# Kernel optimization log

Hardware: AMD Instinct MI355X
Metric: run time of the kernel (lower is better)

## Reference

```python
import jax, jax.numpy as jnp
import numpy as np

B, T, E, H = 4, 8192, 1024, 16
D = E // H
SCALE = 1.0 / np.sqrt(D).astype(np.float32)
EPS_FM = 1e-6
EPS_Z = 1e-8


def setup_inputs() -> dict:
    key = jax.random.key(0)
    ks = jax.random.split(key, 11)
    s = 1.0 / np.sqrt(E).astype(np.float32)  # small init so feature map stays sane
    return {
        'query': jax.random.normal(ks[0], (B, T, E), jnp.float32),
        'key': jax.random.normal(ks[1], (B, T, E), jnp.float32),
        'value': jax.random.normal(ks[2], (B, T, E), jnp.float32),
        'Wq': jax.random.normal(ks[3], (E, E), jnp.float32) * s,
        'bq': jax.random.normal(ks[4], (E,), jnp.float32) * 0.01,
        'Wk': jax.random.normal(ks[5], (E, E), jnp.float32) * s,
        'bk': jax.random.normal(ks[6], (E,), jnp.float32) * 0.01,
        'Wv': jax.random.normal(ks[7], (E, E), jnp.float32) * s,
        'bv': jax.random.normal(ks[8], (E,), jnp.float32) * 0.01,
        'Wo': jax.random.normal(ks[9], (E, E), jnp.float32) * s,
        'bo': jax.random.normal(ks[10], (E,), jnp.float32) * 0.01,
    }


def _heads(x):
    # (B, T, E) -> (B, H, T, D)
    b, t, _ = x.shape
    return x.reshape(b, t, H, D).transpose(0, 2, 1, 3)


def _feature_map(x):
    return jax.nn.relu(x) + EPS_FM


def reference(query, key, value, Wq, bq, Wk, bk, Wv, bv, Wo, bo):
    b, tq, _ = query.shape
    Q = _feature_map(_heads(query @ Wq.T + bq) * SCALE)  # (B,H,Tq,D)
    K = _feature_map(_heads(key @ Wk.T + bk) * SCALE)    # (B,H,Tk,D)
    V = _heads(value @ Wv.T + bv)                         # (B,H,Tk,D)
    KV = jnp.einsum('bhnd,bhne->bhde', K, V)              # (B,H,D,D)
    K_sum = K.sum(axis=2)                                 # (B,H,D)
    Z = jnp.einsum('bhnd,bhd->bhn', Q, K_sum) + EPS_Z     # (B,H,Tq)
    out = jnp.einsum('bhnd,bhde->bhne', Q, KV) / Z[..., None]
    out = out.transpose(0, 2, 1, 3).reshape(b, tq, E)
    return out @ Wo.T + bo
```

## Files before the change

### kernel.cpp

```cpp
#include <hip/hip_runtime.h>
#include <hip/hip_bf16.h>


#define SCALE_ 0.125f
#define EPS_FM_ 1e-6f
#define EPS_Z_ 1e-8f

typedef __bf16 bf16;
typedef __attribute__((ext_vector_type(4))) __bf16 bf16x4;
typedef __attribute__((ext_vector_type(8))) __bf16 bf16x8;
typedef __attribute__((ext_vector_type(8))) unsigned short u16x8;
typedef __attribute__((ext_vector_type(4))) float f32x4;

__device__ __forceinline__ void gl_lds16(const void* g, void* l) {
  __builtin_amdgcn_global_load_lds(
      (const __attribute__((address_space(1))) void*)g,
      (__attribute__((address_space(3))) void*)l, 16, 0, 0);
}

#define SBAR()                                  \
  do {                                          \
    __builtin_amdgcn_sched_barrier(0);          \
    asm volatile("s_barrier" ::: "memory");     \
    __builtin_amdgcn_sched_barrier(0);          \
  } while (0)

__global__ __launch_bounds__(256) void cast_weights(
    const float* __restrict__ Wq, const float* __restrict__ Wk,
    const float* __restrict__ Wv, const float* __restrict__ Wo,
    bf16* __restrict__ out) {
  int which = blockIdx.y;
  int j = (blockIdx.x * 256 + threadIdx.x) * 4;
  const float* s = (which == 0) ? Wq : (which == 1) ? Wk : (which == 2) ? Wv : Wo;
  float4 v = *(const float4*)(s + j);
  bf16x4 p = {(bf16)v.x, (bf16)v.y, (bf16)v.z, (bf16)v.w};
  *(bf16x4*)(out + (size_t)which * (1u << 20) + j) = p;
}

template <int MODE>
__global__ __launch_bounds__(512, 2) void gemm8p(
    const bf16* __restrict__ Ab, const float* __restrict__ Aq,
    const float* __restrict__ Ak, const float* __restrict__ Av,
    const bf16* __restrict__ Wb, const float* __restrict__ b0,
    const float* __restrict__ b1, const float* __restrict__ b2,
    bf16* __restrict__ Pb, float* __restrict__ Pf) {
  __shared__ __align__(16) char lds[65536];
  const int tid = threadIdx.x;
  const int bid = blockIdx.x;
  const int wg = (bid & 7) * (gridDim.x >> 3) + (bid >> 3);
  const int mt = wg >> 2;
  int seg = 0, om = 2;
  if constexpr (MODE == 0) {
    seg = mt >> 7;
    om = (seg < 2) ? 0 : 1;
  }
  const int m0 = (MODE == 0 ? (mt & 127) : mt) * 256;
  const int n0 = (wg & 3) * 256;
  const int wave = tid >> 6, lane = tid & 63;
  const int wm = wave >> 2, wn = wave & 3;
  const int l16 = lane & 15, kg = lane >> 4;
  const int e = l16 & 7;
  const int sw0 = (kg ^ e) << 4;
  const int sw1 = ((4 | kg) ^ e) << 4;

  const int tr = tid >> 3;
  const int cslot = (tid & 7) ^ (tr & 7);
  const bf16* pA = nullptr;
  const float* pAf = nullptr;
  if constexpr (MODE == 1)
    pA = Ab + (size_t)(m0 + tr) * 1024 + cslot * 8;
  else {
    const float* Af = (seg == 0) ? Aq : (seg == 1) ? Ak : Av;
    pAf = Af + (size_t)(m0 + tr) * 1024 + cslot * 8;
  }
  const bf16* W = (MODE == 0) ? Wb + ((size_t)seg << 20) : Wb;
  const float* bias = (MODE == 0) ? ((seg == 0) ? b0 : (seg == 1) ? b1 : b2) : b0;
  const bf16* pB = W + (size_t)(n0 + ((tr >> 5) << 6) + (tr & 31)) * 1024 + cslot * 8;
  char* sA = lds;
  char* sB = lds + 32768;

  auto stgA = [&](int h, int kt) {
    const bf16* g = pA + h * 65536 + kt * 64;
    char* d = sA + h * 16384 + tid * 16;
    gl_lds16(g, d);
    gl_lds16(g + 131072, d + 8192);
  };
  auto stgB = [&](int h, int kt) {
    const bf16* g = pB + h * 32768 + kt * 64;
    char* d = sB + h * 16384 + tid * 16;
    gl_lds16(g, d);
    gl_lds16(g + 131072, d + 8192);
  };
  auto ldgA = [&](int h, int kt, f32x4* r) {
    const float* g = pAf + h * 65536 + kt * 64;
    r[0] = *(const f32x4*)g;
    r[1] = *(const f32x4*)(g + 4);
    r[2] = *(const f32x4*)(g + 131072);
    r[3] = *(const f32x4*)(g + 131072 + 4);
  };
  auto wrA = [&](int h, const f32x4* r) {
    bf16x8 p0 = {(bf16)r[0][0], (bf16)r[0][1], (bf16)r[0][2], (bf16)r[0][3],
                 (bf16)r[1][0], (bf16)r[1][1], (bf16)r[1][2], (bf16)r[1][3]};
    bf16x8 p1 = {(bf16)r[2][0], (bf16)r[2][1], (bf16)r[2][2], (bf16)r[2][3],
                 (bf16)r[3][0], (bf16)r[3][1], (bf16)r[3][2], (bf16)r[3][3]};
    char* d = sA + h * 16384 + tid * 16;
    *(bf16x8*)d = p0;
    *(bf16x8*)(d + 8192) = p1;
  };

  const int aBase = wm * 8192 + l16 * 128;
  const int bBase = wn * 4096 + l16 * 128;
  auto ldA = [&](int h, int fmi, int kk) {
    return *(const bf16x8*)(sA + h * 16384 + aBase + fmi * 2048 +
                            (kk ? sw1 : sw0));
  };
  auto ldB = [&](int h, int fnj, int kk) {
    return *(const bf16x8*)(sB + h * 16384 + bBase + fnj * 2048 +
                            (kk ? sw1 : sw0));
  };

  f32x4 acc[8][4] = {};
  bf16x8 rA[4][2], rB01[2][2], rB23[2][2];
  f32x4 ga[4], gb[4];
  const int NT = 16;

  if constexpr (MODE == 1) {
    stgA(0, 0); stgB(0, 0); stgB(1, 0); stgA(1, 0);
    asm volatile("s_waitcnt vmcnt(2)" ::: "memory");
  } else {
    ldgA(0, 0, ga); ldgA(1, 0, gb);
    stgB(0, 0); stgB(1, 0);
    asm volatile("s_waitcnt vmcnt(12)" ::: "memory");
    wrA(0, ga);
    asm volatile("s_waitcnt vmcnt(4)" ::: "memory");
    wrA(1, gb);
    ldgA(0, 1, ga); ldgA(1, 1, gb);
    asm volatile("s_waitcnt vmcnt(16)" ::: "memory");
    asm volatile("s_waitcnt lgkmcnt(0)" ::: "memory");
  }
  SBAR();

#pragma unroll 2
  for (int t = 0; t < NT; ++t) {
#pragma unroll
    for (int fmi = 0; fmi < 4; ++fmi) {
      rA[fmi][0] = ldA(0, fmi, 0);
      rA[fmi][1] = ldA(0, fmi, 1);
    }
#pragma unroll
    for (int fnj = 0; fnj < 2; ++fnj) {
      rB01[fnj][0] = ldB(0, fnj, 0);
      rB01[fnj][1] = ldB(0, fnj, 1);
    }
    SBAR();
    __builtin_amdgcn_s_setprio(1);
#pragma unroll
    for (int fmi = 0; fmi < 4; ++fmi)
#pragma unroll
      for (int fnj = 0; fnj < 2; ++fnj)
#pragma unroll
        for (int kk = 0; kk < 2; ++kk)
          acc[fmi][fnj] = __builtin_amdgcn_mfma_f32_16x16x32_bf16(
              rA[fmi][kk], rB01[fnj][kk], acc[fmi][fnj], 0, 0, 0);
    __builtin_amdgcn_s_setprio(0);
    SBAR();
#pragma unroll
    for (int fnj = 0; fnj < 2; ++fnj) {
      rB23[fnj][0] = ldB(1, fnj, 0);
      rB23[fnj][1] = ldB(1, fnj, 1);
    }
    if (t + 1 < NT) {
      if constexpr (MODE == 1) stgA(0, t + 1);
      stgB(0, t + 1);
    }
    SBAR();
    __builtin_amdgcn_s_setprio(1);
#pragma unroll
    for (int fmi = 0; fmi < 4; ++fmi)
#pragma unroll
      for (int fnj = 0; fnj < 2; ++fnj)
#pragma unroll
        for (int kk = 0; kk < 2; ++kk)
          acc[fmi][2 + fnj] = __builtin_amdgcn_mfma_f32_16x16x32_bf16(
              rA[fmi][kk], rB23[fnj][kk], acc[fmi][2 + fnj], 0, 0, 0);
    __builtin_amdgcn_s_setprio(0);
    __builtin_amdgcn_sched_barrier(0);
    if constexpr (MODE == 1) {
      if (t + 1 < NT)
        asm volatile("s_waitcnt vmcnt(4)" ::: "memory");
      else
        asm volatile("s_waitcnt vmcnt(0)" ::: "memory");
    }
    SBAR();
#pragma unroll
    for (int fmi = 0; fmi < 4; ++fmi) {
      rA[fmi][0] = ldA(1, fmi, 0);
      rA[fmi][1] = ldA(1, fmi, 1);
    }
    if (t + 1 < NT) stgB(1, t + 1);
    SBAR();
    __builtin_amdgcn_s_setprio(1);
#pragma unroll
    for (int fmi = 0; fmi < 4; ++fmi)
#pragma unroll
      for (int fnj = 0; fnj < 2; ++fnj)
#pragma unroll
        for (int kk = 0; kk < 2; ++kk)
          acc[4 + fmi][2 + fnj] = __builtin_amdgcn_mfma_f32_16x16x32_bf16(
              rA[fmi][kk], rB23[fnj][kk], acc[4 + fmi][2 + fnj], 0, 0, 0);
    __builtin_amdgcn_s_setprio(0);
    __builtin_amdgcn_sched_barrier(0);
    if constexpr (MODE == 0) {
      if (t + 1 < NT) {
        wrA(0, ga);
        if (t + 2 < NT) ldgA(0, t + 2, ga);
      }
    }
    SBAR();
    if constexpr (MODE == 1) {
      if (t + 1 < NT) stgA(1, t + 1);
    }
    SBAR();
    __builtin_amdgcn_s_setprio(1);
#pragma unroll
    for (int fmi = 0; fmi < 4; ++fmi)
#pragma unroll
      for (int fnj = 0; fnj < 2; ++fnj)
#pragma unroll
        for (int kk = 0; kk < 2; ++kk)
          acc[4 + fmi][fnj] = __builtin_amdgcn_mfma_f32_16x16x32_bf16(
              rA[fmi][kk], rB01[fnj][kk], acc[4 + fmi][fnj], 0, 0, 0);
    __builtin_amdgcn_s_setprio(0);
    __builtin_amdgcn_sched_barrier(0);
    if constexpr (MODE == 0) {
      if (t + 1 < NT) {
        wrA(1, gb);
        if (t + 2 < NT) ldgA(1, t + 2, gb);
        if (t + 2 < NT)
          asm volatile("s_waitcnt vmcnt(16)" ::: "memory");
        else
          asm volatile("s_waitcnt vmcnt(0)" ::: "memory");
      }
    } else {
      if (t + 1 < NT)
        asm volatile("s_waitcnt vmcnt(2)" ::: "memory");
    }
    SBAR();
  }

  if constexpr (MODE == 0) {
    bf16* PbS = Pb + (size_t)seg * 33554432u;
#pragma unroll
    for (int hk = 0; hk < 2; ++hk) {
      if (wm == hk) {
#pragma unroll
        for (int fn = 0; fn < 4; ++fn) {
          const int col = wn * 64 + fn * 16 + l16;
          const float bv = bias[n0 + col];
#pragma unroll
          for (int fm = 0; fm < 8; ++fm) {
            const int rl0 = fm * 16 + kg * 4;
#pragma unroll
            for (int i = 0; i < 4; ++i) {
              float v = acc[fm][fn][i] + bv;
              if (om == 0) { v *= SCALE_; v = fmaxf(v, 0.f) + EPS_FM_; }
              const int rl = rl0 + i;
              bf16 bvv = (bf16)v;
              *(unsigned short*)(lds + rl * 512 + ((((col >> 3) ^ (rl & 7))) << 4) +
                                 (col & 7) * 2) =
                  __builtin_bit_cast(unsigned short, bvv);
            }
          }
        }
      }
      __syncthreads();
#pragma unroll
      for (int it = 0; it < 8; ++it) {
        const int gi = it * 512 + tid;
        const int row = gi >> 5, g = gi & 31;
        bf16x8 v = *(const bf16x8*)(lds + row * 512 + ((g ^ (row & 7)) << 4));
        *(bf16x8*)(PbS + (size_t)(m0 + hk * 128 + row) * 1024 + n0 + g * 8) = v;
      }
      __syncthreads();
    }
  } else {
#pragma unroll
    for (int fn = 0; fn < 4; ++fn) {
      const int col = n0 + wn * 64 + fn * 16 + l16;
      const float bv = bias[col];
#pragma unroll
      for (int fm = 0; fm < 8; ++fm) {
        const int row = m0 + wm * 128 + fm * 16 + kg * 4;
#pragma unroll
        for (int i = 0; i < 4; ++i)
          Pf[(size_t)(row + i) * 1024 + col] = acc[fm][fn][i] + bv;
      }
    }
  }
}

__global__ __launch_bounds__(256) void kv_mfma(
    const bf16* __restrict__ Kp, const bf16* __restrict__ Vp,
    float* __restrict__ KVpart, float* __restrict__ KsumPart) {
  __shared__ __align__(16) char lds[65536];
  char* Kt = lds;
  char* Vt = lds + 32768;
  const int bh = blockIdx.x, split = blockIdx.y;
  const int b = bh >> 4, h = bh & 15;
  const int tid = threadIdx.x;
  const int p = tid >> 3, c = tid & 7;
  const int wave = tid >> 6, lane = tid & 63;
  const int wd = wave >> 1, we = wave & 1;
  const int l16 = lane & 15, kg = lane >> 4;
  f32x4 acc[2][2] = {};
  f32x4 accz[2] = {};
  const bf16x8 ones = {1.f, 1.f, 1.f, 1.f, 1.f, 1.f, 1.f, 1.f};

  for (int o = 0; o < 4; ++o) {
    const size_t gbase =
        (size_t)(b * 8192 + split * 1024 + o * 256) * 1024 + h * 64 + c * 8;
    __syncthreads();
#pragma unroll
    for (int i = 0; i < 4; ++i) {
      const int t = i * 64 + p * 2;
      const size_t ga = gbase + (size_t)t * 1024;
      bf16x8 k0 = *(const bf16x8*)(Kp + ga);
      bf16x8 k1 = *(const bf16x8*)(Kp + ga + 1024);
      bf16x8 v0 = *(const bf16x8*)(Vp + ga);
      bf16x8 v1 = *(const bf16x8*)(Vp + ga + 1024);
      u16x8 a0 = __builtin_bit_cast(u16x8, k0);
      u16x8 a1 = __builtin_bit_cast(u16x8, k1);
      u16x8 b0 = __builtin_bit_cast(u16x8, v0);
      u16x8 b1 = __builtin_bit_cast(u16x8, v1);
      const int gt = t >> 3, tl = (t & 7) * 2;
#pragma unroll
      for (int j = 0; j < 8; ++j) {
        const int d = c * 8 + j;
        const int off = d * 512 + ((gt ^ (d & 7) ^ c) << 4) + tl;
        *(unsigned int*)(Kt + off) =
            (unsigned int)a0[j] | ((unsigned int)a1[j] << 16);
        *(unsigned int*)(Vt + off) =
            (unsigned int)b0[j] | ((unsigned int)b1[j] << 16);
      }
    }
    __syncthreads();

#pragma unroll
    for (int ks = 0; ks < 8; ++ks) {
      const int g = ks * 4 + kg;
      bf16x8 af[2], bf_[2];
#pragma unroll
      for (int f = 0; f < 2; ++f) {
        const int d = wd * 32 + f * 16 + l16;
        af[f] = *(const bf16x8*)(Kt + d * 512 +
                                 ((g ^ (d & 7) ^ ((d >> 3) & 7)) << 4));
        const int ee = we * 32 + f * 16 + l16;
        bf_[f] = *(const bf16x8*)(Vt + ee * 512 +
                                  ((g ^ (ee & 7) ^ ((ee >> 3) & 7)) << 4));
      }
#pragma unroll
      for (int fa = 0; fa < 2; ++fa) {
#pragma unroll
        for (int fb = 0; fb < 2; ++fb)
          acc[fa][fb] = __builtin_amdgcn_mfma_f32_16x16x32_bf16(
              af[fa], bf_[fb], acc[fa][fb], 0, 0, 0);
        if (we == 0)
          accz[fa] = __builtin_amdgcn_mfma_f32_16x16x32_bf16(
              af[fa], ones, accz[fa], 0, 0, 0);
      }
    }
  }

  float* outp = KVpart + ((size_t)split * 64 + bh) * 4096;
#pragma unroll
  for (int fa = 0; fa < 2; ++fa)
#pragma unroll
    for (int i = 0; i < 4; ++i) {
      const int d = wd * 32 + fa * 16 + kg * 4 + i;
#pragma unroll
      for (int fb = 0; fb < 2; ++fb)
        outp[d * 64 + we * 32 + fb * 16 + l16] = acc[fa][fb][i];
      if (we == 0 && l16 == 0)
        KsumPart[((size_t)split * 64 + bh) * 64 + d] = accz[fa][i];
    }
}

__global__ __launch_bounds__(256) void kv_reduce(
    const float* __restrict__ KVpart, const float* __restrict__ KsumPart,
    bf16* __restrict__ KVt) {
  int bh = blockIdx.x;
  for (int idx = threadIdx.x; idx < 5120; idx += 256) {
    float s = 0.f;
    if (idx < 4096) {
      int e = idx >> 6, d = idx & 63;
      for (int sp = 0; sp < 8; ++sp)
        s += KVpart[((size_t)sp * 64 + bh) * 4096 + d * 64 + e];
    } else if (idx < 4160) {
      int d = idx - 4096;
      for (int sp = 0; sp < 8; ++sp)
        s += KsumPart[((size_t)sp * 64 + bh) * 64 + d];
    }
    KVt[(size_t)bh * 5120 + idx] = (bf16)s;
  }
}

__global__ __launch_bounds__(256) void attn(
    const bf16* __restrict__ KVt, bf16* __restrict__ QA) {
  __shared__ __align__(16) char lds[43008];
  char* Qt = lds;
  char* Bt = lds + 32768;
  const int bh = blockIdx.x, tc = blockIdx.y;
  const int b = bh >> 4, h = bh & 15;
  const int tid = threadIdx.x;
  const int m0 = b * 8192 + tc * 256;

#pragma unroll
  for (int i = 0; i < 8; ++i) {
    const int gidx = i * 256 + tid;
    const int row = gidx >> 3, g = gidx & 7;
    const int gsrc = g ^ (row & 7);
    gl_lds16(QA + (size_t)(m0 + row) * 1024 + h * 64 + gsrc * 8, Qt + gidx * 16);
  }
#pragma unroll
  for (int i = 0; i < 3; ++i) {
    const int gidx = i * 256 + tid;
    if (gidx < 640) {
      const int row = gidx >> 3, g = gidx & 7;
      const int gsrc = g ^ (row & 7);
      gl_lds16(KVt + (size_t)bh * 5120 + row * 64 + gsrc * 8, Bt + gidx * 16);
    }
  }
  __syncthreads();

  const int wave = tid >> 6, lane = tid & 63;
  const int l16 = lane & 15, kg = lane >> 4;
  bf16x8 a[4][2];
#pragma unroll
  for (int fm = 0; fm < 4; ++fm)
#pragma unroll
    for (int kk = 0; kk < 2; ++kk) {
      const int row = wave * 64 + fm * 16 + l16;
      const int g = kk * 4 + kg;
      a[fm][kk] = *(const bf16x8*)(Qt + row * 128 + ((g ^ (row & 7)) << 4));
    }
  f32x4 acc[4][4] = {};
  f32x4 accz[4] = {};
#pragma unroll
  for (int kk = 0; kk < 2; ++kk) {
    const int g = kk * 4 + kg;
    const int zr = 64 + l16;
    bf16x8 bz = *(const bf16x8*)(Bt + zr * 128 + ((g ^ (zr & 7)) << 4));
#pragma unroll
    for (int fn = 0; fn < 4; ++fn) {
      const int br = fn * 16 + l16;
      bf16x8 bb = *(const bf16x8*)(Bt + br * 128 + ((g ^ (br & 7)) << 4));
#pragma unroll
      for (int fm = 0; fm < 4; ++fm)
        acc[fm][fn] = __builtin_amdgcn_mfma_f32_16x16x32_bf16(
            a[fm][kk], bb, acc[fm][fn], 0, 0, 0);
    }
#pragma unroll
    for (int fm = 0; fm < 4; ++fm)
      accz[fm] = __builtin_amdgcn_mfma_f32_16x16x32_bf16(
          a[fm][kk], bz, accz[fm], 0, 0, 0);
  }
  __syncthreads();

#pragma unroll
  for (int fm = 0; fm < 4; ++fm)
#pragma unroll
    for (int i = 0; i < 4; ++i) {
      const float z = __shfl(accz[fm][i], (lane & 48), 64) + EPS_Z_;
      const float rz = 1.0f / z;
      const int row = wave * 64 + fm * 16 + kg * 4 + i;
#pragma unroll
      for (int fn = 0; fn < 4; ++fn) {
        const int col = fn * 16 + l16;
        const int gc = col >> 3;
        bf16 v = (bf16)(acc[fm][fn][i] * rz);
        *(unsigned short*)(Qt + row * 128 + ((gc ^ (row & 7)) << 4) + (col & 7) * 2) =
            __builtin_bit_cast(unsigned short, v);
      }
    }
  __syncthreads();

#pragma unroll
  for (int i = 0; i < 8; ++i) {
    const int gidx = i * 256 + tid;
    const int row = gidx >> 3, g = gidx & 7;
    bf16x8 v = *(const bf16x8*)(Qt + row * 128 + ((g ^ (row & 7)) << 4));
    *(bf16x8*)(QA + (size_t)(m0 + row) * 1024 + h * 64 + g * 8) = v;
  }
}

extern "C" void kernel_launch(void* const* d_in, const int* in_sizes, int n_in,
                              void* d_out, int out_size, void* d_ws, size_t ws_size,
                              hipStream_t stream) {
  const float* query = (const float*)d_in[0];
  const float* key = (const float*)d_in[1];
  const float* value = (const float*)d_in[2];
  const float* Wq = (const float*)d_in[3];
  const float* bq = (const float*)d_in[4];
  const float* Wk = (const float*)d_in[5];
  const float* bk = (const float*)d_in[6];
  const float* Wv = (const float*)d_in[7];
  const float* bv = (const float*)d_in[8];
  const float* Wo = (const float*)d_in[9];
  const float* bo = (const float*)d_in[10];
  float* out = (float*)d_out;

  bf16* ws = (bf16*)d_ws;
  bf16* Wqb = ws;
  bf16* Wob = ws + (3u << 20);
  bf16* Qp = ws + (4u << 20);
  bf16* Kp = Qp + 33554432u;
  bf16* Vp = Kp + 33554432u;
  bf16* KVt = Vp + 33554432u;
  float* KVpart = (float*)d_out + 16777216u;
  float* KsumPart = KVpart + 8 * 64 * 4096;

  cast_weights<<<dim3(1024, 4), 256, 0, stream>>>(Wq, Wk, Wv, Wo, Wqb);

  gemm8p<0><<<1536, 512, 0, stream>>>(nullptr, query, key, value, Wqb, bq, bk,
                                      bv, Qp, nullptr);

  kv_mfma<<<dim3(64, 8), 256, 0, stream>>>(Kp, Vp, KVpart, KsumPart);
  kv_reduce<<<64, 256, 0, stream>>>(KVpart, KsumPart, KVt);
  attn<<<dim3(64, 32), 256, 0, stream>>>(KVt, Qp);
  gemm8p<1><<<512, 512, 0, stream>>>(Qp, nullptr, nullptr, nullptr, Wob, bo,
                                     bo, bo, nullptr, out);
}
```

Baseline: 435.1 us.

## Prefetch K/V tiles in registers in kv_mfma, split kv_reduce, tighten waitcnt

kv_mfma now loads the next 256-token K/V chunk into registers right after the LDS write barrier, so global loads overlap with the MFMA work on the current chunk instead of stalling at the top of each iteration. kv_reduce is split across four blocks per head to get more parallelism. The gemm waitcnt thresholds drop from 16 to 8 outstanding loads, which waits for more of the A loads to land before the barrier. Prefetching raises register pressure in kv_mfma, and the stricter waitcnt may add stalls in the projection GEMM.

```diff
diff --git a/kernel.cpp b/kernel.cpp
--- a/kernel.cpp
+++ b/kernel.cpp
@@ -135,7 +135,7 @@
     asm volatile("s_waitcnt vmcnt(4)" ::: "memory");
     wrA(1, gb);
     ldgA(0, 1, ga); ldgA(1, 1, gb);
-    asm volatile("s_waitcnt vmcnt(16)" ::: "memory");
+    asm volatile("s_waitcnt vmcnt(8)" ::: "memory");
     asm volatile("s_waitcnt lgkmcnt(0)" ::: "memory");
   }
   SBAR();
@@ -235,11 +235,12 @@
     if constexpr (MODE == 0) {
       if (t + 1 < NT) {
         wrA(1, gb);
-        if (t + 2 < NT) ldgA(1, t + 2, gb);
-        if (t + 2 < NT)
-          asm volatile("s_waitcnt vmcnt(16)" ::: "memory");
-        else
+        if (t + 2 < NT) {
+          ldgA(1, t + 2, gb);
+          asm volatile("s_waitcnt vmcnt(8)" ::: "memory");
+        } else {
           asm volatile("s_waitcnt vmcnt(0)" ::: "memory");
+        }
       }
     } else {
       if (t + 1 < NT)
@@ -315,23 +316,28 @@
   f32x4 acc[2][2] = {};
   f32x4 accz[2] = {};
   const bf16x8 ones = {1.f, 1.f, 1.f, 1.f, 1.f, 1.f, 1.f, 1.f};
+  const size_t gbase0 =
+      (size_t)(b * 8192 + split * 1024) * 1024 + h * 64 + c * 8;
+
+  bf16x8 pk0[4], pk1[4], pv0[4], pv1[4];
+#pragma unroll
+  for (int i = 0; i < 4; ++i) {
+    const size_t ga = gbase0 + (size_t)(i * 64 + p * 2) * 1024;
+    pk0[i] = *(const bf16x8*)(Kp + ga);
+    pk1[i] = *(const bf16x8*)(Kp + ga + 1024);
+    pv0[i] = *(const bf16x8*)(Vp + ga);
+    pv1[i] = *(const bf16x8*)(Vp + ga + 1024);
+  }
 
   for (int o = 0; o < 4; ++o) {
-    const size_t gbase =
-        (size_t)(b * 8192 + split * 1024 + o * 256) * 1024 + h * 64 + c * 8;
     __syncthreads();
 #pragma unroll
     for (int i = 0; i < 4; ++i) {
       const int t = i * 64 + p * 2;
-      const size_t ga = gbase + (size_t)t * 1024;
-      bf16x8 k0 = *(const bf16x8*)(Kp + ga);
-      bf16x8 k1 = *(const bf16x8*)(Kp + ga + 1024);
-      bf16x8 v0 = *(const bf16x8*)(Vp + ga);
-      bf16x8 v1 = *(const bf16x8*)(Vp + ga + 1024);
-      u16x8 a0 = __builtin_bit_cast(u16x8, k0);
-      u16x8 a1 = __builtin_bit_cast(u16x8, k1);
-      u16x8 b0 = __builtin_bit_cast(u16x8, v0);
-      u16x8 b1 = __builtin_bit_cast(u16x8, v1);
+      u16x8 a0 = __builtin_bit_cast(u16x8, pk0[i]);
+      u16x8 a1 = __builtin_bit_cast(u16x8, pk1[i]);
+      u16x8 b0 = __builtin_bit_cast(u16x8, pv0[i]);
+      u16x8 b1 = __builtin_bit_cast(u16x8, pv1[i]);
       const int gt = t >> 3, tl = (t & 7) * 2;
 #pragma unroll
       for (int j = 0; j < 8; ++j) {
@@ -344,6 +350,16 @@
       }
     }
     __syncthreads();
+    if (o + 1 < 4) {
+#pragma unroll
+      for (int i = 0; i < 4; ++i) {
+        const size_t ga = gbase0 + (size_t)((o + 1) * 256 + i * 64 + p * 2) * 1024;
+        pk0[i] = *(const bf16x8*)(Kp + ga);
+        pk1[i] = *(const bf16x8*)(Kp + ga + 1024);
+        pv0[i] = *(const bf16x8*)(Vp + ga);
+        pv1[i] = *(const bf16x8*)(Vp + ga + 1024);
+      }
+    }
 
 #pragma unroll
     for (int ks = 0; ks < 8; ++ks) {
@@ -388,8 +404,9 @@
 __global__ __launch_bounds__(256) void kv_reduce(
     const float* __restrict__ KVpart, const float* __restrict__ KsumPart,
     bf16* __restrict__ KVt) {
-  int bh = blockIdx.x;
-  for (int idx = threadIdx.x; idx < 5120; idx += 256) {
+  int bh = blockIdx.x >> 2;
+  int q = blockIdx.x & 3;
+  for (int idx = q * 1280 + threadIdx.x; idx < (q + 1) * 1280; idx += 256) {
     float s = 0.f;
     if (idx < 4096) {
       int e = idx >> 6, d = idx & 63;
@@ -525,7 +542,7 @@
                                       bv, Qp, nullptr);
 
   kv_mfma<<<dim3(64, 8), 256, 0, stream>>>(Kp, Vp, KVpart, KsumPart);
-  kv_reduce<<<64, 256, 0, stream>>>(KVpart, KsumPart, KVt);
+  kv_reduce<<<256, 256, 0, stream>>>(KVpart, KsumPart, KVt);
   attn<<<dim3(64, 32), 256, 0, stream>>>(KVt, Qp);
   gemm8p<1><<<512, 512, 0, stream>>>(Qp, nullptr, nullptr, nullptr, Wob, bo,
                                      bo, bo, nullptr, out);
```

New measurement: 428.1 us, median of 3. About the same (-1.6%).
